# Performance work log

Hardware: AMD Instinct MI355X
Metric: run time of the kernel (lower is better)

Reference implementation:

```python
import jax, jax.numpy as jnp
import numpy as np

D_SUMMARY = 128
N_LAYERS = 24
N_HEADS = 16
D_HEAD = 64
HIDDEN = 512
ACTIVE_MIN = 12
ROT = 16
THETA = 10000.0
B, P = 16, 128
L_ACT = N_LAYERS - ACTIVE_MIN
OUT_DIM = N_HEADS * 2 * D_HEAD


def setup_inputs() -> dict:
    key = jax.random.key(0)
    k1, k2, k3, k4, k5, k6 = jax.random.split(key, 6)
    summary_stack = jax.random.normal(k1, (B, P, D_SUMMARY), jnp.float32)
    positions = jnp.sort(jax.random.randint(k2, (P,), 0, 8192))
    s1 = 1.0 / np.sqrt(D_SUMMARY)
    s2 = 1.0 / np.sqrt(HIDDEN)
    W1 = jax.random.uniform(k3, (L_ACT, D_SUMMARY, HIDDEN), jnp.float32, -s1, s1)
    b1 = jax.random.uniform(k4, (L_ACT, HIDDEN), jnp.float32, -s1, s1)
    W2 = jax.random.uniform(k5, (L_ACT, HIDDEN, OUT_DIM), jnp.float32, -s2, s2)
    b2 = jax.random.uniform(k6, (L_ACT, OUT_DIM), jnp.float32, -s2, s2)
    return {"summary_stack": summary_stack, "positions": positions,
            "W1": W1, "b1": b1, "W2": W2, "b2": b2}


def reference(summary_stack, positions, W1, b1, W2, b2):
    # Batched 2-layer MLP across all active layers (grouped GEMM)
    h = jax.nn.relu(jnp.einsum('bps,lsh->lbph', summary_stack, W1) + b1[:, None, None, :])
    kv = jnp.einsum('lbph,lho->lbpo', h, W2) + b2[:, None, None, :]
    kv = kv.reshape(L_ACT, B, P, N_HEADS, 2, D_HEAD)
    k = jnp.transpose(kv[..., 0, :], (0, 1, 3, 2, 4))  # (L,B,H,P,D)
    v = jnp.transpose(kv[..., 1, :], (0, 1, 3, 2, 4))
    # RoPE on first ROT dims of K
    inv_freq = 1.0 / (THETA ** (jnp.arange(0, ROT, 2, dtype=jnp.float32) / ROT))
    freqs = positions.astype(jnp.float32)[:, None] * inv_freq[None, :]  # (P, ROT//2)
    emb = jnp.concatenate([freqs, freqs], axis=-1)  # (P, ROT)
    cos, sin = jnp.cos(emb), jnp.sin(emb)
    k_rot, k_pass = k[..., :ROT], k[..., ROT:]
    rot_half = jnp.concatenate([-k_rot[..., ROT // 2:], k_rot[..., :ROT // 2]], axis=-1)
    k_emb = k_rot * cos + rot_half * sin
    k = jnp.concatenate([k_emb, k_pass], axis=-1)
    # Inactive layers get zero K/V
    zeros = jnp.zeros((ACTIVE_MIN, B, N_HEADS, P, D_HEAD), k.dtype)
    k_all = jnp.concatenate([zeros, k], axis=0)
    v_all = jnp.concatenate([zeros, v], axis=0)
    return jnp.stack([k_all, v_all], axis=1)  # (n_layers, 2, B, H, P, D)
```

## Files before the change

### kernel.cpp

```cpp
#include <hip/hip_runtime.h>
#include <hip/hip_bf16.h>

#define L_ACT   12
#define BDIM    16
#define PDIM    128
#define DSUM    128
#define HID     512
#define ODIM    2048
#define NHEAD   16
#define DHEAD   64
#define MROWS   2048

typedef short s16x4  __attribute__((ext_vector_type(4)));
typedef short short8 __attribute__((ext_vector_type(8)));
typedef float f32x4  __attribute__((ext_vector_type(4)));

__device__ __forceinline__ void gload_lds16(const __hip_bfloat16* g, __hip_bfloat16* l) {
  __builtin_amdgcn_global_load_lds(
      (const __attribute__((address_space(1))) unsigned int*)g,
      (__attribute__((address_space(3))) unsigned int*)l, 16, 0, 0);
}

__device__ __forceinline__ short f2bf(float x) {
  __hip_bfloat16 h = __float2bfloat16(x);
  return *reinterpret_cast<short*>(&h);
}

__global__ __launch_bounds__(256) void zerofill_kernel(f32x4* __restrict__ p, int n16) {
  int stride = gridDim.x * 256;
  for (int i = blockIdx.x * 256 + threadIdx.x; i < n16; i += stride)
    p[i] = {0.f, 0.f, 0.f, 0.f};
}

__global__ __launch_bounds__(256) void prep_tiny(
    const int* __restrict__ positions, const float* __restrict__ W1,
    float* __restrict__ cs, __hip_bfloat16* __restrict__ W1T) {
  const int bid = blockIdx.x;
  const int tid = threadIdx.x;
  if (bid == 768) {
#pragma unroll
    for (int q = 0; q < 4; ++q) {
      int i = q * 256 + tid;
      int p = i >> 3, f = i & 7;
      double inv = pow(10000.0, -(double)f / 8.0);
      double ang = (double)positions[p] * inv;
      cs[i]        = (float)cos(ang);
      cs[1024 + i] = (float)sin(ang);
    }
  } else {
    __shared__ float t[32][33];
    int bx = bid & 15, by = (bid >> 4) & 3, l = bid >> 6;
    int o0 = bx * 32, j0 = by * 32;
    int tx = tid & 31, ty = tid >> 5;
    const float* ip = W1 + (size_t)l * DSUM * HID;
#pragma unroll
    for (int r = 0; r < 32; r += 8)
      t[ty + r][tx] = ip[(size_t)(j0 + ty + r) * HID + o0 + tx];
    __syncthreads();
    __hip_bfloat16* op = W1T + (size_t)l * DSUM * HID;
#pragma unroll
    for (int r = 0; r < 32; r += 8)
      op[(size_t)(o0 + ty + r) * DSUM + j0 + tx] = __float2bfloat16(t[tx][ty + r]);
  }
}

__global__ __launch_bounds__(256) void gemm1_128(
    const float* __restrict__ summary,
    const __hip_bfloat16* __restrict__ Ball,
    const float* __restrict__ bias,
    __hip_bfloat16* __restrict__ Hall,
    const float* __restrict__ W2,
    __hip_bfloat16* __restrict__ W2T,
    f32x4* __restrict__ zeroBase, int doZero) {
  const int KTOT = DSUM, NTOT = HID;
  __shared__ __hip_bfloat16 shbuf[17408];
  __hip_bfloat16* ldsA = shbuf;
  __hip_bfloat16* ldsB = shbuf + 8192;
  const int l    = blockIdx.z;
  const int n0   = blockIdx.x * 128;
  const int m0   = blockIdx.y * 128;
  const int tid  = threadIdx.x;
  const int wid  = tid >> 6;
  const int lane = tid & 63;
  const int wr = wid >> 1, wc = wid & 1;
  const __hip_bfloat16* Bt = Ball + (size_t)l * NTOT * KTOT;

  f32x4 acc[4][4];
#pragma unroll
  for (int m = 0; m < 4; ++m)
#pragma unroll
    for (int n = 0; n < 4; ++n)
      acc[m][n] = {0.f, 0.f, 0.f, 0.f};

  const int srowi = lane >> 3;
  const int sblk  = (lane & 7) ^ srowi;

  for (int kt = 0; kt < KTOT / 64; ++kt) {
    __syncthreads();
#pragma unroll
    for (int s = 0; s < 4; ++s) {
      int seg = wid * 4 + s;
      int row = seg * 8 + srowi;
      gload_lds16(Bt + (size_t)(n0 + row) * KTOT + kt * 64 + sblk * 8, ldsB + seg * 512);
    }
#pragma unroll
    for (int j = 0; j < 8; ++j) {
      int s = j * 256 + tid;
      int r = s >> 4, g = s & 15;
      f32x4 v = *(const f32x4*)(summary + (size_t)(m0 + r) * DSUM + kt * 64 + g * 4);
      s16x4 w;
      w[0] = f2bf(v[0]); w[1] = f2bf(v[1]); w[2] = f2bf(v[2]); w[3] = f2bf(v[3]);
      int ch = g >> 1;
      *(s16x4*)((char*)ldsA + r * 128 + ((ch ^ (r & 7)) << 4) + (g & 1) * 8) = w;
    }
    __syncthreads();
#pragma unroll
    for (int kk = 0; kk < 2; ++kk) {
      short8 af[4], bfr[4];
#pragma unroll
      for (int m = 0; m < 4; ++m) {
        int row = wr * 64 + m * 16 + (lane & 15);
        int off = (kk * 64 + (lane >> 4) * 16) ^ ((row & 7) << 4);
        af[m] = *(const short8*)((const char*)ldsA + row * 128 + off);
      }
#pragma unroll
      for (int n = 0; n < 4; ++n) {
        int row = wc * 64 + n * 16 + (lane & 15);
        int off = (kk * 64 + (lane >> 4) * 16) ^ ((row & 7) << 4);
        bfr[n] = *(const short8*)((const char*)ldsB + row * 128 + off);
      }
#pragma unroll
      for (int m = 0; m < 4; ++m)
#pragma unroll
        for (int n = 0; n < 4; ++n)
          acc[m][n] = __builtin_amdgcn_mfma_f32_16x16x32_bf16(af[m], bfr[n], acc[m][n], 0, 0, 0);
    }
  }

  const int bid = blockIdx.x + 4 * blockIdx.y + 64 * blockIdx.z;

  __syncthreads();
#pragma unroll
  for (int n = 0; n < 4; ++n) {
    int col = wc * 64 + n * 16 + (lane & 15);
    float bb = bias[l * NTOT + n0 + col];
#pragma unroll
    for (int m = 0; m < 4; ++m) {
      int rowb = wr * 64 + m * 16 + ((lane >> 4) << 2);
#pragma unroll
      for (int j = 0; j < 4; ++j) {
        float v = acc[m][n][j] + bb;
        v = v > 0.f ? v : 0.f;
        shbuf[(rowb + j) * 136 + col] = __float2bfloat16(v);
      }
    }
  }
  __syncthreads();
  {
    __hip_bfloat16* H = Hall + (size_t)l * MROWS * HID;
#pragma unroll
    for (int i = 0; i < 8; ++i) {
      int idx = i * 256 + tid;
      int row = idx >> 4, seg = idx & 15;
      short8 v = *(const short8*)(shbuf + row * 136 + seg * 8);
      *(short8*)(H + (size_t)(m0 + row) * HID + n0 + seg * 8) = v;
    }
  }

  {
    float* tb0 = (float*)shbuf;
    float* tb1 = (float*)shbuf + 1056;
    const int tx = tid & 31, ty = tid >> 5;
    const int tbase = bid * 16;
    const f32x4 z = {0.f, 0.f, 0.f, 0.f};
    f32x4* zp = zeroBase + (size_t)bid * 8192;
    float rvA0, rvA1, rvA2, rvA3, rvB0, rvB1, rvB2, rvB3;

#define W2_LOAD(P, tt_) do {                                                \
      int t_ = tbase + (tt_);                                               \
      int lz_ = t_ >> 10, rem_ = t_ & 1023;                                 \
      int j0_ = (rem_ >> 6) * 32, o0_ = (rem_ & 63) * 32;                   \
      const float* ip_ = W2 + (size_t)lz_ * HID * ODIM                      \
                       + (size_t)(j0_ + ty) * ODIM + o0_ + tx;              \
      P##0 = ip_[0];                                                        \
      P##1 = ip_[(size_t)8 * ODIM];                                         \
      P##2 = ip_[(size_t)16 * ODIM];                                        \
      P##3 = ip_[(size_t)24 * ODIM];                                        \
    } while (0)

#define W2_WRITE(buf, P) do {                                               \
      (buf)[(ty +  0) * 33 + tx] = P##0;                                    \
      (buf)[(ty +  8) * 33 + tx] = P##1;                                    \
      (buf)[(ty + 16) * 33 + tx] = P##2;                                    \
      (buf)[(ty + 24) * 33 + tx] = P##3;                                    \
    } while (0)

#define W2_STORE(buf, tt_) do {                                             \
      int t_ = tbase + (tt_);                                               \
      int lz_ = t_ >> 10, rem_ = t_ & 1023;                                 \
      int j0_ = (rem_ >> 6) * 32, o0_ = (rem_ & 63) * 32;                   \
      __hip_bfloat16* op_ = W2T + (size_t)lz_ * HID * ODIM;                 \
      _Pragma("unroll")                                                     \
      for (int r_ = 0; r_ < 4; ++r_)                                        \
        op_[(size_t)(o0_ + ty + 8 * r_) * HID + j0_ + tx] =                 \
            __float2bfloat16((buf)[tx * 33 + ty + 8 * r_]);                 \
    } while (0)

#define ZCHUNK(tt_) do { if (doZero && (tt_) < 8) {                         \
      _Pragma("unroll")                                                     \
      for (int q_ = 0; q_ < 4; ++q_)                                        \
        __builtin_nontemporal_store(z, zp + ((tt_) * 4 + q_) * 256 + tid);  \
    } } while (0)

    W2_LOAD(rvA, 0);
    W2_LOAD(rvB, 1);
    W2_WRITE(tb0, rvA);
    __syncthreads();
#pragma unroll 1
    for (int tt = 0; tt < 16; tt += 2) {
      if (tt + 2 < 16) W2_LOAD(rvA, tt + 2);
      W2_STORE(tb0, tt);
      W2_WRITE(tb1, rvB);
      ZCHUNK(tt);
      __syncthreads();
      if (tt + 3 < 16) W2_LOAD(rvB, tt + 3);
      W2_STORE(tb1, tt + 1);
      if (tt + 2 < 16) W2_WRITE(tb0, rvA);
      ZCHUNK(tt + 1);
      __syncthreads();
    }
#undef W2_LOAD
#undef W2_WRITE
#undef W2_STORE
#undef ZCHUNK
  }
}

__global__ __launch_bounds__(256, 2) void gemm2_pipe(
    const __hip_bfloat16* __restrict__ Aall,
    const __hip_bfloat16* __restrict__ Ball,
    const float* __restrict__ bias,
    const float* __restrict__ cs,
    float* __restrict__ O,
    f32x4* __restrict__ zeroBase, int doZero) {
  __shared__ __hip_bfloat16 lds[3 * 12288];
  const int orig = blockIdx.x + 16 * blockIdx.y + 128 * blockIdx.z;
  const int nw   = (orig & 7) * 192 + (orig >> 3);
  const int bx   = nw & 15;
  const int by   = (nw >> 4) & 7;
  const int l    = nw >> 7;
  const int n0  = bx * 128;
  const int m0  = by * 256;
  const int tid = threadIdx.x;
  const int wid = tid >> 6, lane = tid & 63;
  const int wm  = wid >> 1, wn = wid & 1;
  const __hip_bfloat16* A  = Aall + (size_t)l * MROWS * HID;
  const __hip_bfloat16* Bt = Ball + (size_t)l * ODIM * HID;
  f32x4* zq = zeroBase + (size_t)nw * 4096;
  const f32x4 zv = {0.f, 0.f, 0.f, 0.f};

  f32x4 acc[8][4];
#pragma unroll
  for (int m = 0; m < 8; ++m)
#pragma unroll
    for (int n = 0; n < 4; ++n)
      acc[m][n] = {0.f, 0.f, 0.f, 0.f};

  int ra[4], ca[4], rb[2], cb[2];
#pragma unroll
  for (int j = 0; j < 4; ++j) {
    int cx = j * 256 + tid;
    ra[j] = cx >> 2; ca[j] = (cx & 3) ^ ((ra[j] >> 1) & 3);
  }
#pragma unroll
  for (int j = 0; j < 2; ++j) {
    int cx = j * 256 + tid;
    rb[j] = cx >> 2; cb[j] = (cx & 3) ^ ((rb[j] >> 1) & 3);
  }

#define STAGE_A(slot, kt) do {                                                      \
    _Pragma("unroll")                                                               \
    for (int j_ = 0; j_ < 4; ++j_)                                                  \
      gload_lds16(A + (size_t)(m0 + ra[j_]) * HID + (kt) * 32 + ca[j_] * 8,         \
                  lds + (slot) * 12288 + j_ * 2048 + wid * 512);                    \
  } while (0)
#define STAGE_B(slot, kt) do {                                                      \
    _Pragma("unroll")                                                               \
    for (int j_ = 0; j_ < 2; ++j_)                                                  \
      gload_lds16(Bt + (size_t)(n0 + rb[j_]) * HID + (kt) * 32 + cb[j_] * 8,        \
                  lds + (slot) * 12288 + 8192 + j_ * 2048 + wid * 512);             \
  } while (0)

  const int kq   = lane >> 4;
  const int rl15 = lane & 15;

#define LD_FRAG(dst, base, rr) do {                                                 \
    int r_ = (rr);                                                                  \
    int off_ = r_ * 64 + ((kq ^ ((r_ >> 1) & 3)) << 4);                             \
    dst = *(const short8*)((const char*)(base) + off_);                             \
  } while (0)

  STAGE_A(0, 0); STAGE_B(0, 0);
  STAGE_A(1, 1); STAGE_B(1, 1);
  asm volatile("s_waitcnt vmcnt(6)" ::: "memory");
  __builtin_amdgcn_s_barrier();

  const int NT = HID / 32;
  for (int t = 0; t < NT; ++t) {
    const int cur = t % 3;
    const __hip_bfloat16* sa = lds + cur * 12288;
    const __hip_bfloat16* sb = sa + 8192;
    short8 af[4], bfr[4];

    if (doZero)
      __builtin_nontemporal_store(zv, zq + t * 256 + tid);

#pragma unroll
    for (int n = 0; n < 4; ++n) LD_FRAG(bfr[n], sb, wn * 64 + n * 16 + rl15);
#pragma unroll
    for (int mi = 0; mi < 4; ++mi) LD_FRAG(af[mi], sa, wm * 128 + mi * 16 + rl15);
    if (t + 2 < NT) STAGE_A((t + 2) % 3, t + 2);
    __builtin_amdgcn_s_barrier();
    __builtin_amdgcn_s_setprio(1);
#pragma unroll
    for (int mi = 0; mi < 4; ++mi)
#pragma unroll
      for (int n = 0; n < 4; ++n)
        acc[mi][n] = __builtin_amdgcn_mfma_f32_16x16x32_bf16(af[mi], bfr[n], acc[mi][n], 0, 0, 0);
    __builtin_amdgcn_s_setprio(0);
    __builtin_amdgcn_s_barrier();

#pragma unroll
    for (int mi = 0; mi < 4; ++mi) LD_FRAG(af[mi], sa, wm * 128 + 64 + mi * 16 + rl15);
    if (t + 2 < NT) STAGE_B((t + 2) % 3, t + 2);
    __builtin_amdgcn_s_barrier();
    __builtin_amdgcn_s_setprio(1);
#pragma unroll
    for (int mi = 0; mi < 4; ++mi)
#pragma unroll
      for (int n = 0; n < 4; ++n)
        acc[4 + mi][n] = __builtin_amdgcn_mfma_f32_16x16x32_bf16(af[mi], bfr[n], acc[4 + mi][n], 0, 0, 0);
    __builtin_amdgcn_s_setprio(0);
    if (t < NT - 2)       asm volatile("s_waitcnt vmcnt(6)" ::: "memory");
    else if (t == NT - 2) asm volatile("s_waitcnt vmcnt(0)" ::: "memory");
    __builtin_amdgcn_s_barrier();
  }
#undef STAGE_A
#undef STAGE_B
#undef LD_FRAG

  __syncthreads();
  const int head = bx;
  const int tkv  = wn;
  const int bidx = by * 2 + wm;
  float* slab = O + ((((size_t)(l + L_ACT) * 2 + tkv) * BDIM + bidx) * NHEAD + head) * (PDIM * DHEAD);
  const bool ropeWave = (tkv == 0);

  float bb[4];
#pragma unroll
  for (int n = 0; n < 4; ++n) bb[n] = bias[l * ODIM + n0 + wn * 64 + n * 16 + rl15];

  float* Tw = (float*)lds + wid * 2080;

#pragma unroll
  for (int c = 0; c < 4; ++c) {
#pragma unroll
    for (int mh = 0; mh < 2; ++mh) {
      int mf = c * 2 + mh;
      int pl = mh * 16 + (lane >> 4) * 4;
#pragma unroll
      for (int n = 0; n < 4; ++n) {
#pragma unroll
        for (int j = 0; j < 4; ++j) {
          float v = acc[mf][n][j] + bb[n];
          if (ropeWave && n == 0) {
            float partner = __shfl_xor(v, 8);
            int p = c * 32 + pl + j;
            float cv = cs[p * 8 + (lane & 7)];
            float sv = cs[1024 + p * 8 + (lane & 7)];
            v = v * cv + (((lane & 15) < 8) ? -partner : partner) * sv;
          }
          Tw[(pl + j) * 65 + n * 16 + rl15] = v;
        }
      }
    }
#pragma unroll
    for (int it = 0; it < 8; ++it) {
      int pl = it * 4 + (lane >> 4);
      f32x4 vv = *(const f32x4*)(Tw + pl * 65 + rl15 * 4);
      __builtin_nontemporal_store(vv, (f32x4*)(slab + (size_t)(c * 32 + pl) * DHEAD + rl15 * 4));
    }
  }
}

extern "C" void kernel_launch(void* const* d_in, const int* in_sizes, int n_in,
                              void* d_out, int out_size, void* d_ws, size_t ws_size,
                              hipStream_t stream) {
  const float* summary   = (const float*)d_in[0];
  const int*   positions = (const int*)d_in[1];
  const float* W1 = (const float*)d_in[2];
  const float* b1 = (const float*)d_in[3];
  const float* W2 = (const float*)d_in[4];
  const float* b2 = (const float*)d_in[5];
  float* out = (float*)d_out;

  const size_t SCRATCH_BYTES = 25165824ULL + 25165824ULL + 1572864ULL + 8192ULL;
  const bool useWs = (ws_size >= SCRATCH_BYTES);
  char* sc = useWs ? (char*)d_ws : (char*)d_out;
  __hip_bfloat16* h_bf = (__hip_bfloat16*)sc;
  __hip_bfloat16* W2T  = (__hip_bfloat16*)(sc + 25165824);
  __hip_bfloat16* W1T  = (__hip_bfloat16*)(sc + 50331648);
  float*          cs   = (float*)(sc + 51904512);

  prep_tiny<<<769, 256, 0, stream>>>(positions, W1, cs, W1T);

  gemm1_128<<<dim3(HID / 128, MROWS / 128, L_ACT), 256, 0, stream>>>(
      summary, W1T, b1, h_bf, W2, W2T,
      (f32x4*)((char*)d_out + 100663296), useWs ? 1 : 0);
  gemm2_pipe<<<dim3(ODIM / 128, MROWS / 256, L_ACT), 256, 0, stream>>>(
      h_bf, W2T, b2, cs, out, (f32x4*)d_out, useWs ? 1 : 0);

  if (!useWs)
    zerofill_kernel<<<2048, 256, 0, stream>>>((f32x4*)d_out, 12582912);
}
```

Measured before the change: 126.7 us.

## Fuse W1 transpose/convert and RoPE table into gemm1, drop prep kernel

Removes the separate prep_tiny launch. Each gemm1 block now loads its 128-column W1 slice straight from fp32, converts it to bf16 and stores it transposed and swizzled in LDS. Block 0 also computes the cos/sin table. This drops one kernel launch and the W1T round trip through global memory. In exchange each block does strided fp32 reads of W1, the 64 blocks sharing a (layer, n0) slice repeat the same conversion, and LDS use grows to 48KB.

```diff
diff --git a/kernel.cpp b/kernel.cpp
--- a/kernel.cpp
+++ b/kernel.cpp
@@ -32,12 +32,30 @@
     p[i] = {0.f, 0.f, 0.f, 0.f};
 }
 
-__global__ __launch_bounds__(256) void prep_tiny(
-    const int* __restrict__ positions, const float* __restrict__ W1,
-    float* __restrict__ cs, __hip_bfloat16* __restrict__ W1T) {
-  const int bid = blockIdx.x;
-  const int tid = threadIdx.x;
-  if (bid == 768) {
+__global__ __launch_bounds__(256) void gemm1_128(
+    const float* __restrict__ summary,
+    const float* __restrict__ W1,
+    const int*   __restrict__ positions,
+    const float* __restrict__ bias,
+    __hip_bfloat16* __restrict__ Hall,
+    const float* __restrict__ W2,
+    __hip_bfloat16* __restrict__ W2T,
+    float* __restrict__ cs,
+    f32x4* __restrict__ zeroBase, int doZero) {
+  const int KTOT = DSUM, NTOT = HID;
+  __shared__ __hip_bfloat16 shbuf[24576];
+  __hip_bfloat16* ldsB2 = shbuf;
+  __hip_bfloat16* ldsA  = shbuf + 16384;
+  const int l    = blockIdx.z;
+  const int n0   = blockIdx.x * 128;
+  const int m0   = blockIdx.y * 128;
+  const int tid  = threadIdx.x;
+  const int wid  = tid >> 6;
+  const int lane = tid & 63;
+  const int wr = wid >> 1, wc = wid & 1;
+  const int bid = blockIdx.x + 4 * blockIdx.y + 64 * blockIdx.z;
+
+  if (bid == 0) {
 #pragma unroll
     for (int q = 0; q < 4; ++q) {
       int i = q * 256 + tid;
@@ -47,43 +65,23 @@
       cs[i]        = (float)cos(ang);
       cs[1024 + i] = (float)sin(ang);
     }
-  } else {
-    __shared__ float t[32][33];
-    int bx = bid & 15, by = (bid >> 4) & 3, l = bid >> 6;
-    int o0 = bx * 32, j0 = by * 32;
-    int tx = tid & 31, ty = tid >> 5;
-    const float* ip = W1 + (size_t)l * DSUM * HID;
-#pragma unroll
-    for (int r = 0; r < 32; r += 8)
-      t[ty + r][tx] = ip[(size_t)(j0 + ty + r) * HID + o0 + tx];
-    __syncthreads();
-    __hip_bfloat16* op = W1T + (size_t)l * DSUM * HID;
-#pragma unroll
-    for (int r = 0; r < 32; r += 8)
-      op[(size_t)(o0 + ty + r) * DSUM + j0 + tx] = __float2bfloat16(t[tx][ty + r]);
-  }
-}
-
-__global__ __launch_bounds__(256) void gemm1_128(
-    const float* __restrict__ summary,
-    const __hip_bfloat16* __restrict__ Ball,
-    const float* __restrict__ bias,
-    __hip_bfloat16* __restrict__ Hall,
-    const float* __restrict__ W2,
-    __hip_bfloat16* __restrict__ W2T,
-    f32x4* __restrict__ zeroBase, int doZero) {
-  const int KTOT = DSUM, NTOT = HID;
-  __shared__ __hip_bfloat16 shbuf[17408];
-  __hip_bfloat16* ldsA = shbuf;
-  __hip_bfloat16* ldsB = shbuf + 8192;
-  const int l    = blockIdx.z;
-  const int n0   = blockIdx.x * 128;
-  const int m0   = blockIdx.y * 128;
-  const int tid  = threadIdx.x;
-  const int wid  = tid >> 6;
-  const int lane = tid & 63;
-  const int wr = wid >> 1, wc = wid & 1;
-  const __hip_bfloat16* Bt = Ball + (size_t)l * NTOT * KTOT;
+  }
+
+  {
+    const float* Wp = W1 + (size_t)l * DSUM * HID + n0;
+#pragma unroll
+    for (int q = 0; q < 16; ++q) {
+      int g  = q * 256 + tid;
+      int j4 = g >> 7;
+      int r  = g & 127;
+      s16x4 w;
+#pragma unroll
+      for (int jj = 0; jj < 4; ++jj)
+        w[jj] = f2bf(Wp[(size_t)(j4 * 4 + jj) * HID + r]);
+      int chunk = (j4 >> 1) ^ (r & 7);
+      *(s16x4*)((char*)ldsB2 + r * 256 + chunk * 16 + (j4 & 1) * 8) = w;
+    }
+  }
 
   f32x4 acc[4][4];
 #pragma unroll
@@ -92,17 +90,10 @@
     for (int n = 0; n < 4; ++n)
       acc[m][n] = {0.f, 0.f, 0.f, 0.f};
 
-  const int srowi = lane >> 3;
-  const int sblk  = (lane & 7) ^ srowi;
+  const int kq = lane >> 4;
 
   for (int kt = 0; kt < KTOT / 64; ++kt) {
     __syncthreads();
-#pragma unroll
-    for (int s = 0; s < 4; ++s) {
-      int seg = wid * 4 + s;
-      int row = seg * 8 + srowi;
-      gload_lds16(Bt + (size_t)(n0 + row) * KTOT + kt * 64 + sblk * 8, ldsB + seg * 512);
-    }
 #pragma unroll
     for (int j = 0; j < 8; ++j) {
       int s = j * 256 + tid;
@@ -120,14 +111,14 @@
 #pragma unroll
       for (int m = 0; m < 4; ++m) {
         int row = wr * 64 + m * 16 + (lane & 15);
-        int off = (kk * 64 + (lane >> 4) * 16) ^ ((row & 7) << 4);
+        int off = (kk * 64 + kq * 16) ^ ((row & 7) << 4);
         af[m] = *(const short8*)((const char*)ldsA + row * 128 + off);
       }
 #pragma unroll
       for (int n = 0; n < 4; ++n) {
         int row = wc * 64 + n * 16 + (lane & 15);
-        int off = (kk * 64 + (lane >> 4) * 16) ^ ((row & 7) << 4);
-        bfr[n] = *(const short8*)((const char*)ldsB + row * 128 + off);
+        int chunk = (kt * 8 + kk * 4 + kq) ^ (row & 7);
+        bfr[n] = *(const short8*)((const char*)ldsB2 + row * 256 + chunk * 16);
       }
 #pragma unroll
       for (int m = 0; m < 4; ++m)
@@ -136,8 +127,6 @@
           acc[m][n] = __builtin_amdgcn_mfma_f32_16x16x32_bf16(af[m], bfr[n], acc[m][n], 0, 0, 0);
     }
   }
-
-  const int bid = blockIdx.x + 4 * blockIdx.y + 64 * blockIdx.z;
 
   __syncthreads();
 #pragma unroll
@@ -166,6 +155,7 @@
       *(short8*)(H + (size_t)(m0 + row) * HID + n0 + seg * 8) = v;
     }
   }
+  __syncthreads();
 
   {
     float* tb0 = (float*)shbuf;
@@ -404,18 +394,15 @@
   const float* b2 = (const float*)d_in[5];
   float* out = (float*)d_out;
 
-  const size_t SCRATCH_BYTES = 25165824ULL + 25165824ULL + 1572864ULL + 8192ULL;
+  const size_t SCRATCH_BYTES = 25165824ULL + 25165824ULL + 8192ULL;
   const bool useWs = (ws_size >= SCRATCH_BYTES);
   char* sc = useWs ? (char*)d_ws : (char*)d_out;
   __hip_bfloat16* h_bf = (__hip_bfloat16*)sc;
   __hip_bfloat16* W2T  = (__hip_bfloat16*)(sc + 25165824);
-  __hip_bfloat16* W1T  = (__hip_bfloat16*)(sc + 50331648);
-  float*          cs   = (float*)(sc + 51904512);
-
-  prep_tiny<<<769, 256, 0, stream>>>(positions, W1, cs, W1T);
+  float*          cs   = (float*)(sc + 50331648);
 
   gemm1_128<<<dim3(HID / 128, MROWS / 128, L_ACT), 256, 0, stream>>>(
-      summary, W1T, b1, h_bf, W2, W2T,
+      summary, W1, positions, b1, h_bf, W2, W2T, cs,
       (f32x4*)((char*)d_out + 100663296), useWs ? 1 : 0);
   gemm2_pipe<<<dim3(ODIM / 128, MROWS / 256, L_ACT), 256, 0, stream>>>(
       h_bf, W2T, b2, cs, out, (f32x4*)d_out, useWs ? 1 : 0);
```

New measurement: 124.4 us. No clear change (-1.8%).
